# Optimization experiments

Hardware: AMD Instinct MI355X
Metric: run time of the kernel (lower is better)

## Reference

```python
import jax, jax.numpy as jnp
import numpy as np

N, E, IN, H, D = 50000, 800000, 128, 2, 64  # nodes, edges, in_dim, heads, out_dim per head
EPS = 1e-16  # PyG softmax denominator epsilon


def setup_inputs() -> dict:
    key = jax.random.key(0)
    ks = jax.random.split(key, 10)
    s = 1.0 / np.sqrt(IN)
    u = lambda k, shape: jax.random.uniform(k, shape, jnp.float32, -s, s)
    return {
        "x": jax.random.normal(ks[0], (N, IN), jnp.float32),
        "edge_index": jax.random.randint(ks[1], (2, E), 0, N, jnp.int64),
        "Wq": u(ks[2], (IN, H * D)), "bq": u(ks[3], (H * D,)),
        "Wk": u(ks[4], (IN, H * D)), "bk": u(ks[5], (H * D,)),
        "Wv": u(ks[6], (IN, H * D)), "bv": u(ks[7], (H * D,)),
        "Ws": u(ks[8], (IN, H * D)), "bs": u(ks[9], (H * D,)),
    }


def reference(x, edge_index, Wq, bq, Wk, bk, Wv, bv, Ws, bs):
    src, dst = edge_index[0], edge_index[1]
    # node-level projections [N, H, D]
    q = (x @ Wq + bq).reshape(N, H, D)
    k = (x @ Wk + bk).reshape(N, H, D)
    v = (x @ Wv + bv).reshape(N, H, D)
    # per-edge attention logits [E, H]
    alpha = jnp.einsum('ehd,ehd->eh', q[dst], k[src]) / np.float32(np.sqrt(D))
    # segment softmax over incoming edges of each dst node
    amax = jax.ops.segment_max(alpha, dst, num_segments=N)      # [N, H]
    amax = jnp.where(jnp.isfinite(amax), amax, 0.0)
    ealpha = jnp.exp(alpha - amax[dst])                          # [E, H]
    denom = jax.ops.segment_sum(ealpha, dst, num_segments=N)     # [N, H]
    w = ealpha / (denom[dst] + EPS)                              # [E, H]
    # scatter-aggregate weighted values -> [N, H, D]
    agg = jax.ops.segment_sum(w[:, :, None] * v[src], dst, num_segments=N)
    out = agg.reshape(N, H * D) + (x @ Ws + bs)                  # root/skip term
    return jax.nn.relu(out)
```

## Files before the change

kernel.cpp:

```cpp
#include <hip/hip_runtime.h>
#include <hip/hip_bf16.h>


#define N_NODES 50000
#define E_EDGES 800000
#define IN_DIM  128
#define HD      128
#define NPB     256
#define NB      196
#define EB      2048
#define NBLK_AC ((E_EDGES + EB - 1) / EB)
#define NTILES  ((N_NODES + 63) / 64)
#define PBLK    256
#define PSCALE  0.18033688011112042f

typedef float  f32x4  __attribute__((ext_vector_type(4)));
typedef float  f32x2  __attribute__((ext_vector_type(2)));
typedef __bf16 bf16x8 __attribute__((ext_vector_type(8)));
typedef unsigned short u16x8 __attribute__((ext_vector_type(8)));

__device__ __forceinline__ float bf2f(unsigned short u) {
    return __uint_as_float((unsigned int)u << 16);
}

__global__ __launch_bounds__(512) void proj_kernel(
    const float* __restrict__ x,
    const float* __restrict__ Wq, const float* __restrict__ bq,
    const float* __restrict__ Wk, const float* __restrict__ bk,
    const float* __restrict__ Wv, const float* __restrict__ bv,
    const float* __restrict__ Ws, const float* __restrict__ bs,
    __bf16* __restrict__ qb, unsigned char* __restrict__ kv8,
    __bf16* __restrict__ sbuf)
{
    __shared__ __bf16 xs[64][136];

    const int tid  = threadIdx.x;
    const int lane = tid & 63;
    const int wave = tid >> 6;
    const int l15  = lane & 15;
    const int g    = lane >> 4;

    const int p    = wave >> 1;
    const int colh = (wave & 1) * 64;
    const float* Wp     = (p == 0) ? Wq : (p == 1) ? Wk : (p == 2) ? Wv : Ws;
    const float* bias_p = (p == 0) ? bq : (p == 1) ? bk : (p == 2) ? bv : bs;

    bf16x8 Bf[4][4];
    #pragma unroll
    for (int ks = 0; ks < 4; ++ks) {
        #pragma unroll
        for (int cf = 0; cf < 4; ++cf) {
            bf16x8 b;
            #pragma unroll
            for (int j = 0; j < 8; ++j)
                b[j] = (__bf16)Wp[(size_t)(ks * 32 + g * 8 + j) * HD + colh + cf * 16 + l15];
            Bf[ks][cf] = b;
        }
    }

    float bias_v[4];
    #pragma unroll
    for (int cf = 0; cf < 4; ++cf) bias_v[cf] = bias_p[colh + cf * 16 + l15];

    const int srow = tid >> 5;
    const int sc4  = tid & 31;

    int t = blockIdx.x;
    float4 pre[4];
    if (t < NTILES) {
        #pragma unroll
        for (int it = 0; it < 4; ++it) {
            int row  = it * 16 + srow;
            int grow = t * 64 + row;
            pre[it] = (grow < N_NODES) ? *(const float4*)(x + (size_t)grow * IN_DIM + sc4 * 4)
                                       : make_float4(0.f, 0.f, 0.f, 0.f);
        }
    }

    for (; t < NTILES; t += PBLK) {
        __syncthreads();
        #pragma unroll
        for (int it = 0; it < 4; ++it) {
            int row = it * 16 + srow;
            __bf16* dst = &xs[row][sc4 * 4];
            dst[0] = (__bf16)pre[it].x; dst[1] = (__bf16)pre[it].y;
            dst[2] = (__bf16)pre[it].z; dst[3] = (__bf16)pre[it].w;
        }
        __syncthreads();

        int tn = t + PBLK;
        if (tn < NTILES) {
            #pragma unroll
            for (int it = 0; it < 4; ++it) {
                int row  = it * 16 + srow;
                int grow = tn * 64 + row;
                pre[it] = (grow < N_NODES) ? *(const float4*)(x + (size_t)grow * IN_DIM + sc4 * 4)
                                           : make_float4(0.f, 0.f, 0.f, 0.f);
            }
        }

        f32x4 acc[4][4];
        #pragma unroll
        for (int i = 0; i < 4; ++i)
            #pragma unroll
            for (int j = 0; j < 4; ++j) acc[i][j] = (f32x4){0.f, 0.f, 0.f, 0.f};

        #pragma unroll
        for (int ks = 0; ks < 4; ++ks) {
            #pragma unroll
            for (int rf = 0; rf < 4; ++rf) {
                bf16x8 A = *(const bf16x8*)&xs[rf * 16 + l15][ks * 32 + g * 8];
                #pragma unroll
                for (int cf = 0; cf < 4; ++cf)
                    acc[rf][cf] = __builtin_amdgcn_mfma_f32_16x16x32_bf16(A, Bf[ks][cf], acc[rf][cf], 0, 0, 0);
            }
        }

        const int nodebase = t * 64;
        if (p == 0 || p == 3) {
            __bf16* outp = (p == 0) ? qb : sbuf;
            #pragma unroll
            for (int cf = 0; cf < 4; ++cf) {
                int col = colh + cf * 16 + l15;
                #pragma unroll
                for (int rf = 0; rf < 4; ++rf) {
                    #pragma unroll
                    for (int r = 0; r < 4; ++r) {
                        int grow = nodebase + rf * 16 + g * 4 + r;
                        if (grow < N_NODES)
                            outp[(size_t)grow * HD + col] = (__bf16)(acc[rf][cf][r] + bias_v[cf]);
                    }
                }
            }
        } else {
            unsigned char* outp = kv8 + ((p == 2) ? 128 : 0);
            #pragma unroll
            for (int cf = 0; cf < 4; ++cf) {
                int col = colh + cf * 16 + l15;
                #pragma unroll
                for (int rf = 0; rf < 4; ++rf) {
                    #pragma unroll
                    for (int r = 0; r < 4; ++r) {
                        int grow = nodebase + rf * 16 + g * 4 + r;
                        if (grow < N_NODES) {
                            float val = acc[rf][cf][r] + bias_v[cf];
                            unsigned int pk = __builtin_amdgcn_cvt_pk_fp8_f32(val, val, 0, false);
                            outp[(size_t)grow * 256 + col] = (unsigned char)(pk & 0xff);
                        }
                    }
                }
            }
        }
    }
}

__global__ __launch_bounds__(256) void histA(
    const int* __restrict__ ei, int* __restrict__ hist)
{
    __shared__ int h[NB];
    const int tid = threadIdx.x;
    for (int i = tid; i < NB; i += 256) h[i] = 0;
    __syncthreads();

    const int* dsts = ei + E_EDGES;
    const int base = blockIdx.x * EB;
    #pragma unroll
    for (int half = 0; half < 2; ++half) {
        int e0 = base + half * 1024 + tid * 4;
        if (e0 + 3 < E_EDGES) {
            int4 d = *(const int4*)(dsts + e0);
            atomicAdd(&h[d.x >> 8], 1);
            atomicAdd(&h[d.y >> 8], 1);
            atomicAdd(&h[d.z >> 8], 1);
            atomicAdd(&h[d.w >> 8], 1);
        } else {
            for (int j = 0; j < 4; ++j)
                if (e0 + j < E_EDGES) atomicAdd(&h[dsts[e0 + j] >> 8], 1);
        }
    }
    __syncthreads();
    for (int i = tid; i < NB; i += 256)
        hist[i * NBLK_AC + blockIdx.x] = h[i];
}

__global__ __launch_bounds__(256) void scanB1(
    int* __restrict__ hist, int* __restrict__ sums)
{
    __shared__ int a[512];
    const int tid = threadIdx.x;
    const int b   = blockIdx.x;
    int* hb = hist + (size_t)b * NBLK_AC;

    a[tid]       = (tid       < NBLK_AC) ? hb[tid]       : 0;
    a[tid + 256] = (tid + 256 < NBLK_AC) ? hb[tid + 256] : 0;
    __syncthreads();
    #pragma unroll
    for (int d = 1; d < 512; d <<= 1) {
        int v0 = a[tid],       u0 = (tid       >= d) ? a[tid - d]       : 0;
        int v1 = a[tid + 256], u1 = (tid + 256 >= d) ? a[tid + 256 - d] : 0;
        __syncthreads();
        a[tid] = v0 + u0; a[tid + 256] = v1 + u1;
        __syncthreads();
    }
    if (tid < NBLK_AC)       hb[tid]       = (tid == 0) ? 0 : a[tid - 1];
    if (tid + 256 < NBLK_AC) hb[tid + 256] = a[tid + 255];
    if (tid == 0) sums[b] = a[NBLK_AC - 1];
}

__global__ __launch_bounds__(256) void scanB2(
    const int* __restrict__ sums, int* __restrict__ binbase)
{
    __shared__ int a[256];
    const int tid = threadIdx.x;
    a[tid] = (tid < NB) ? sums[tid] : 0;
    __syncthreads();
    #pragma unroll
    for (int d = 1; d < 256; d <<= 1) {
        int v = a[tid];
        int u = (tid >= d) ? a[tid - d] : 0;
        __syncthreads();
        a[tid] = v + u;
        __syncthreads();
    }
    if (tid < NB) binbase[tid] = (tid == 0) ? 0 : a[tid - 1];
    if (tid == 0) binbase[NB] = a[255];
}

__global__ __launch_bounds__(256) void scatterC(
    const int* __restrict__ ei, const int* __restrict__ hist,
    const int* __restrict__ binbase, int2* __restrict__ part)
{
    __shared__ int hb[NB];
    __shared__ int h2[NB];
    const int tid = threadIdx.x;
    for (int i = tid; i < NB; i += 256) {
        hb[i] = hist[i * NBLK_AC + blockIdx.x] + binbase[i];
        h2[i] = 0;
    }
    __syncthreads();

    const int* srcs = ei;
    const int* dsts = ei + E_EDGES;
    const int base = blockIdx.x * EB;
    #pragma unroll
    for (int half = 0; half < 2; ++half) {
        int e0 = base + half * 1024 + tid * 4;
        if (e0 + 3 < E_EDGES) {
            int4 s4 = *(const int4*)(srcs + e0);
            int4 d4 = *(const int4*)(dsts + e0);
            int bin, r;
            bin = d4.x >> 8; r = atomicAdd(&h2[bin], 1); part[hb[bin] + r] = make_int2(s4.x, d4.x);
            bin = d4.y >> 8; r = atomicAdd(&h2[bin], 1); part[hb[bin] + r] = make_int2(s4.y, d4.y);
            bin = d4.z >> 8; r = atomicAdd(&h2[bin], 1); part[hb[bin] + r] = make_int2(s4.z, d4.z);
            bin = d4.w >> 8; r = atomicAdd(&h2[bin], 1); part[hb[bin] + r] = make_int2(s4.w, d4.w);
        } else {
            for (int j = 0; j < 4; ++j) {
                if (e0 + j < E_EDGES) {
                    int sv = srcs[e0 + j], dv = dsts[e0 + j];
                    int bin = dv >> 8;
                    int r = atomicAdd(&h2[bin], 1);
                    part[hb[bin] + r] = make_int2(sv, dv);
                }
            }
        }
    }
}

__global__ __launch_bounds__(256) void buildD(
    const int2* __restrict__ part, const int* __restrict__ binbase,
    int* __restrict__ slot, int* __restrict__ nbase)
{
    __shared__ int cnt2[NPB];
    __shared__ int pfx[NPB];
    __shared__ int ofs[NPB];
    const int tid = threadIdx.x;
    const int b   = blockIdx.x;
    const int lo  = binbase[b];
    const int hi  = binbase[b + 1];
    const int n0  = b * NPB;

    cnt2[tid] = 0;
    __syncthreads();
    for (int i = lo + tid; i < hi; i += 256)
        atomicAdd(&cnt2[part[i].y - n0], 1);
    __syncthreads();

    pfx[tid] = cnt2[tid];
    __syncthreads();
    #pragma unroll
    for (int d = 1; d < NPB; d <<= 1) {
        int v = pfx[tid];
        int u = (tid >= d) ? pfx[tid - d] : 0;
        __syncthreads();
        pfx[tid] = v + u;
        __syncthreads();
    }
    const int excl = pfx[tid] - cnt2[tid];
    ofs[tid] = excl;
    const int node = n0 + tid;
    if (node < N_NODES) nbase[node] = lo + excl;
    if (b == NB - 1 && tid == 0) nbase[N_NODES] = E_EDGES;
    __syncthreads();

    for (int i = lo + tid; i < hi; i += 256) {
        int2 e = part[i];
        int r = atomicAdd(&ofs[e.y - n0], 1);
        slot[lo + r] = e.x;
    }
}

__global__ __launch_bounds__(256) void aggregate_kernel(
    const __bf16* __restrict__ qb, const unsigned char* __restrict__ kv8,
    const __bf16* __restrict__ sbuf,
    const int* __restrict__ nbase, const int* __restrict__ slot,
    float* __restrict__ out)
{
    const int tid  = threadIdx.x;
    const int lane = tid & 63;
    const int wave = tid >> 6;
    const int h    = lane >> 5;
    const int lh   = lane & 31;
    const int s    = lh >> 4;
    const int l16  = lh & 15;
    const int node = blockIdx.x * 8 + wave * 2 + h;
    const bool nvalid = node < N_NODES;
    const int nc = nvalid ? node : 0;

    const int bse = nbase[nc];
    const int deg = nvalid ? (nbase[nc + 1] - bse) : 0;

    u16x8 qu = *(const u16x8*)(qb + (size_t)nc * HD + 8 * l16);
    float qf[8];
    #pragma unroll
    for (int c = 0; c < 8; ++c) qf[c] = bf2f(qu[c]);

    float lsum = 0.f;
    float acc[8];
    #pragma unroll
    for (int c = 0; c < 8; ++c) acc[c] = 0.f;

    for (int i = 0; i < deg; i += 8) {
        int  jj[4], se[4];
        uint2 kr[4], vr[4];
        float d[4];

        #pragma unroll
        for (int r = 0; r < 4; ++r) {
            jj[r] = i + 2 * r + s;
            int sv = slot[bse + ((jj[r] < deg) ? jj[r] : 0)];
            se[r] = (jj[r] < deg) ? sv : 0;
        }
        #pragma unroll
        for (int r = 0; r < 4; ++r) {
            const unsigned char* rowp = kv8 + (size_t)se[r] * 256 + 8 * l16;
            kr[r] = *(const uint2*)rowp;
            vr[r] = *(const uint2*)(rowp + 128);
        }
        #pragma unroll
        for (int r = 0; r < 4; ++r) {
            f32x2 ka = __builtin_amdgcn_cvt_pk_f32_fp8(kr[r].x, 0);
            f32x2 kb_ = __builtin_amdgcn_cvt_pk_f32_fp8(kr[r].x, 1);
            f32x2 kc = __builtin_amdgcn_cvt_pk_f32_fp8(kr[r].y, 0);
            f32x2 kd = __builtin_amdgcn_cvt_pk_f32_fp8(kr[r].y, 1);
            d[r] = qf[0] * ka.x + qf[1] * ka.y + qf[2] * kb_.x + qf[3] * kb_.y
                 + qf[4] * kc.x + qf[5] * kc.y + qf[6] * kd.x + qf[7] * kd.y;
        }
        #pragma unroll
        for (int m = 1; m <= 4; m <<= 1) {
            d[0] += __shfl_xor(d[0], m);
            d[1] += __shfl_xor(d[1], m);
            d[2] += __shfl_xor(d[2], m);
            d[3] += __shfl_xor(d[3], m);
        }
        #pragma unroll
        for (int r = 0; r < 4; ++r) {
            float a2 = (jj[r] < deg) ? d[r] * PSCALE : -INFINITY;
            float p  = exp2f(a2);
            lsum += p;
            f32x2 va = __builtin_amdgcn_cvt_pk_f32_fp8(vr[r].x, 0);
            f32x2 vb_ = __builtin_amdgcn_cvt_pk_f32_fp8(vr[r].x, 1);
            f32x2 vc = __builtin_amdgcn_cvt_pk_f32_fp8(vr[r].y, 0);
            f32x2 vd = __builtin_amdgcn_cvt_pk_f32_fp8(vr[r].y, 1);
            acc[0] += p * va.x;  acc[1] += p * va.y;
            acc[2] += p * vb_.x; acc[3] += p * vb_.y;
            acc[4] += p * vc.x;  acc[5] += p * vc.y;
            acc[6] += p * vd.x;  acc[7] += p * vd.y;
        }
    }

    lsum += __shfl_xor(lsum, 16);
    #pragma unroll
    for (int c = 0; c < 8; ++c) acc[c] += __shfl_xor(acc[c], 16);

    float inv = (deg > 0) ? 1.f / (lsum + 1e-16f) : 0.f;
    u16x8 su = *(const u16x8*)(sbuf + (size_t)nc * HD + 8 * l16);

    f32x4 ov;
    #pragma unroll
    for (int cc = 0; cc < 4; ++cc) {
        float av;
        unsigned short sv;
        switch (cc) {
            case 0: av = s ? acc[4] : acc[0]; sv = s ? su[4] : su[0]; break;
            case 1: av = s ? acc[5] : acc[1]; sv = s ? su[5] : su[1]; break;
            case 2: av = s ? acc[6] : acc[2]; sv = s ? su[6] : su[2]; break;
            default: av = s ? acc[7] : acc[3]; sv = s ? su[7] : su[3]; break;
        }
        ov[cc] = fmaxf(av * inv + bf2f(sv), 0.f);
    }
    if (nvalid)
        *(f32x4*)(out + (size_t)node * HD + 8 * l16 + 4 * s) = ov;
}

extern "C" void kernel_launch(void* const* d_in, const int* in_sizes, int n_in,
                              void* d_out, int out_size, void* d_ws, size_t ws_size,
                              hipStream_t stream)
{
    const float* x  = (const float*)d_in[0];
    const int*   ei = (const int*)d_in[1];
    const float* Wq = (const float*)d_in[2];
    const float* bq = (const float*)d_in[3];
    const float* Wk = (const float*)d_in[4];
    const float* bk = (const float*)d_in[5];
    const float* Wv = (const float*)d_in[6];
    const float* bv = (const float*)d_in[7];
    const float* Ws = (const float*)d_in[8];
    const float* bs = (const float*)d_in[9];

    char* ws = (char*)d_ws;
    size_t off = 0;
    auto alloc = [&](size_t bytes) {
        void* p = ws + off;
        off += (bytes + 255) & ~(size_t)255;
        return p;
    };
    const size_t projB = (size_t)N_NODES * HD * sizeof(__bf16);
    __bf16* qb = (__bf16*)alloc(projB);
    unsigned char* kv8 = (unsigned char*)alloc((size_t)N_NODES * 256);
    __bf16* sbf = (__bf16*)alloc(projB);
    int* hist    = (int*)alloc((size_t)NB * NBLK_AC * sizeof(int));
    int* sums    = (int*)alloc((size_t)NB * sizeof(int));
    int* binbase = (int*)alloc((size_t)(NB + 1) * sizeof(int));
    int2* part   = (int2*)alloc((size_t)E_EDGES * sizeof(int2));
    int* slot    = (int*)alloc((size_t)E_EDGES * sizeof(int));
    int* nbase   = (int*)alloc((size_t)(N_NODES + 1) * sizeof(int));

    histA<<<NBLK_AC, 256, 0, stream>>>(ei, hist);
    scanB1<<<NB, 256, 0, stream>>>(hist, sums);
    scanB2<<<1, 256, 0, stream>>>(sums, binbase);
    scatterC<<<NBLK_AC, 256, 0, stream>>>(ei, hist, binbase, part);
    buildD<<<NB, 256, 0, stream>>>(part, binbase, slot, nbase);

    proj_kernel<<<PBLK, 512, 0, stream>>>(
        x, Wq, bq, Wk, bk, Wv, bv, Ws, bs, qb, kv8, sbf);

    aggregate_kernel<<<(N_NODES + 7) / 8, 256, 0, stream>>>(
        qb, kv8, sbf, nbase, slot, (float*)d_out);
}
```

Baseline: 90.97 us.

## Restructure projection into single-wave blocks with pre-transposed bf16 weights

Adds a small kernel that transposes all four weight matrices to bf16 so each wave can load its B fragments as vector loads instead of 8 strided scalar fp32 loads. The projection kernel becomes 4096 one-wave blocks, each owning one projection/column-half role. Each wave reads 16-row x tiles straight from global memory into registers, with no LDS staging and no barriers. The cost is that every x tile is now read by 8 different waves instead of once per block, which leans on L2, and it adds an extra kernel launch.

```diff
diff --git a/kernel.cpp b/kernel.cpp
--- a/kernel.cpp
+++ b/kernel.cpp
@@ -10,8 +10,8 @@
 #define NB      196
 #define EB      2048
 #define NBLK_AC ((E_EDGES + EB - 1) / EB)
-#define NTILES  ((N_NODES + 63) / 64)
-#define PBLK    256
+#define NT16    (N_NODES / 16)
+#define PWAVES  4096
 #define PSCALE  0.18033688011112042f
 
 typedef float  f32x4  __attribute__((ext_vector_type(4)));
@@ -23,113 +23,81 @@
     return __uint_as_float((unsigned int)u << 16);
 }
 
-__global__ __launch_bounds__(512) void proj_kernel(
-    const float* __restrict__ x,
-    const float* __restrict__ Wq, const float* __restrict__ bq,
-    const float* __restrict__ Wk, const float* __restrict__ bk,
-    const float* __restrict__ Wv, const float* __restrict__ bv,
-    const float* __restrict__ Ws, const float* __restrict__ bs,
+__global__ __launch_bounds__(256) void wtrans_kernel(
+    const float* __restrict__ Wq, const float* __restrict__ Wk,
+    const float* __restrict__ Wv, const float* __restrict__ Ws,
+    __bf16* __restrict__ WT)
+{
+    int idx = blockIdx.x * 256 + threadIdx.x;
+    int p   = idx >> 14;
+    int rem = idx & 16383;
+    int k   = rem >> 7;
+    int col = rem & 127;
+    const float* W = (p == 0) ? Wq : (p == 1) ? Wk : (p == 2) ? Wv : Ws;
+    WT[(size_t)p * 16384 + col * 128 + k] = (__bf16)W[k * HD + col];
+}
+
+__global__ __launch_bounds__(64) void proj_kernel(
+    const float* __restrict__ x, const __bf16* __restrict__ WT,
+    const float* __restrict__ bq, const float* __restrict__ bk,
+    const float* __restrict__ bv, const float* __restrict__ bs,
     __bf16* __restrict__ qb, unsigned char* __restrict__ kv8,
     __bf16* __restrict__ sbuf)
 {
-    __shared__ __bf16 xs[64][136];
-
-    const int tid  = threadIdx.x;
-    const int lane = tid & 63;
-    const int wave = tid >> 6;
+    const int lane = threadIdx.x & 63;
     const int l15  = lane & 15;
     const int g    = lane >> 4;
 
-    const int p    = wave >> 1;
-    const int colh = (wave & 1) * 64;
-    const float* Wp     = (p == 0) ? Wq : (p == 1) ? Wk : (p == 2) ? Wv : Ws;
+    const int role = blockIdx.x & 7;
+    const int p    = role >> 1;
+    const int colh = (role & 1) * 64;
+
     const float* bias_p = (p == 0) ? bq : (p == 1) ? bk : (p == 2) ? bv : bs;
+    const __bf16* WTp = WT + ((size_t)p * 128 + colh) * 128;
 
     bf16x8 Bf[4][4];
     #pragma unroll
-    for (int ks = 0; ks < 4; ++ks) {
-        #pragma unroll
-        for (int cf = 0; cf < 4; ++cf) {
-            bf16x8 b;
+    for (int ks = 0; ks < 4; ++ks)
+        #pragma unroll
+        for (int cf = 0; cf < 4; ++cf)
+            Bf[ks][cf] = *(const bf16x8*)(WTp + (size_t)(cf * 16 + l15) * 128 + ks * 32 + g * 8);
+
+    float bias_v[4];
+    #pragma unroll
+    for (int cf = 0; cf < 4; ++cf) bias_v[cf] = bias_p[colh + cf * 16 + l15];
+
+    for (int t = blockIdx.x >> 3; t < NT16; t += (PWAVES >> 3)) {
+        const float* xrow = x + (size_t)(t * 16 + l15) * IN_DIM;
+
+        bf16x8 A[4];
+        #pragma unroll
+        for (int ks = 0; ks < 4; ++ks) {
+            f32x4 a0 = *(const f32x4*)(xrow + ks * 32 + g * 8);
+            f32x4 a1 = *(const f32x4*)(xrow + ks * 32 + g * 8 + 4);
+            bf16x8 a;
+            a[0] = (__bf16)a0.x; a[1] = (__bf16)a0.y; a[2] = (__bf16)a0.z; a[3] = (__bf16)a0.w;
+            a[4] = (__bf16)a1.x; a[5] = (__bf16)a1.y; a[6] = (__bf16)a1.z; a[7] = (__bf16)a1.w;
+            A[ks] = a;
+        }
+
+        f32x4 acc[4];
+        #pragma unroll
+        for (int cf = 0; cf < 4; ++cf) acc[cf] = (f32x4){0.f, 0.f, 0.f, 0.f};
+        #pragma unroll
+        for (int ks = 0; ks < 4; ++ks)
             #pragma unroll
-            for (int j = 0; j < 8; ++j)
-                b[j] = (__bf16)Wp[(size_t)(ks * 32 + g * 8 + j) * HD + colh + cf * 16 + l15];
-            Bf[ks][cf] = b;
-        }
-    }
-
-    float bias_v[4];
-    #pragma unroll
-    for (int cf = 0; cf < 4; ++cf) bias_v[cf] = bias_p[colh + cf * 16 + l15];
-
-    const int srow = tid >> 5;
-    const int sc4  = tid & 31;
-
-    int t = blockIdx.x;
-    float4 pre[4];
-    if (t < NTILES) {
-        #pragma unroll
-        for (int it = 0; it < 4; ++it) {
-            int row  = it * 16 + srow;
-            int grow = t * 64 + row;
-            pre[it] = (grow < N_NODES) ? *(const float4*)(x + (size_t)grow * IN_DIM + sc4 * 4)
-                                       : make_float4(0.f, 0.f, 0.f, 0.f);
-        }
-    }
-
-    for (; t < NTILES; t += PBLK) {
-        __syncthreads();
-        #pragma unroll
-        for (int it = 0; it < 4; ++it) {
-            int row = it * 16 + srow;
-            __bf16* dst = &xs[row][sc4 * 4];
-            dst[0] = (__bf16)pre[it].x; dst[1] = (__bf16)pre[it].y;
-            dst[2] = (__bf16)pre[it].z; dst[3] = (__bf16)pre[it].w;
-        }
-        __syncthreads();
-
-        int tn = t + PBLK;
-        if (tn < NTILES) {
-            #pragma unroll
-            for (int it = 0; it < 4; ++it) {
-                int row  = it * 16 + srow;
-                int grow = tn * 64 + row;
-                pre[it] = (grow < N_NODES) ? *(const float4*)(x + (size_t)grow * IN_DIM + sc4 * 4)
-                                           : make_float4(0.f, 0.f, 0.f, 0.f);
-            }
-        }
-
-        f32x4 acc[4][4];
-        #pragma unroll
-        for (int i = 0; i < 4; ++i)
-            #pragma unroll
-            for (int j = 0; j < 4; ++j) acc[i][j] = (f32x4){0.f, 0.f, 0.f, 0.f};
-
-        #pragma unroll
-        for (int ks = 0; ks < 4; ++ks) {
-            #pragma unroll
-            for (int rf = 0; rf < 4; ++rf) {
-                bf16x8 A = *(const bf16x8*)&xs[rf * 16 + l15][ks * 32 + g * 8];
-                #pragma unroll
-                for (int cf = 0; cf < 4; ++cf)
-                    acc[rf][cf] = __builtin_amdgcn_mfma_f32_16x16x32_bf16(A, Bf[ks][cf], acc[rf][cf], 0, 0, 0);
-            }
-        }
-
-        const int nodebase = t * 64;
+            for (int cf = 0; cf < 4; ++cf)
+                acc[cf] = __builtin_amdgcn_mfma_f32_16x16x32_bf16(A[ks], Bf[ks][cf], acc[cf], 0, 0, 0);
+
         if (p == 0 || p == 3) {
             __bf16* outp = (p == 0) ? qb : sbuf;
             #pragma unroll
             for (int cf = 0; cf < 4; ++cf) {
                 int col = colh + cf * 16 + l15;
                 #pragma unroll
-                for (int rf = 0; rf < 4; ++rf) {
-                    #pragma unroll
-                    for (int r = 0; r < 4; ++r) {
-                        int grow = nodebase + rf * 16 + g * 4 + r;
-                        if (grow < N_NODES)
-                            outp[(size_t)grow * HD + col] = (__bf16)(acc[rf][cf][r] + bias_v[cf]);
-                    }
+                for (int r = 0; r < 4; ++r) {
+                    int node = t * 16 + g * 4 + r;
+                    outp[(size_t)node * HD + col] = (__bf16)(acc[cf][r] + bias_v[cf]);
                 }
             }
         } else {
@@ -138,16 +106,11 @@
             for (int cf = 0; cf < 4; ++cf) {
                 int col = colh + cf * 16 + l15;
                 #pragma unroll
-                for (int rf = 0; rf < 4; ++rf) {
-                    #pragma unroll
-                    for (int r = 0; r < 4; ++r) {
-                        int grow = nodebase + rf * 16 + g * 4 + r;
-                        if (grow < N_NODES) {
-                            float val = acc[rf][cf][r] + bias_v[cf];
-                            unsigned int pk = __builtin_amdgcn_cvt_pk_fp8_f32(val, val, 0, false);
-                            outp[(size_t)grow * 256 + col] = (unsigned char)(pk & 0xff);
-                        }
-                    }
+                for (int r = 0; r < 4; ++r) {
+                    int node = t * 16 + g * 4 + r;
+                    float val = acc[cf][r] + bias_v[cf];
+                    unsigned int pk = __builtin_amdgcn_cvt_pk_fp8_f32(val, val, 0, false);
+                    outp[(size_t)node * 256 + col] = (unsigned char)(pk & 0xff);
                 }
             }
         }
@@ -438,6 +401,7 @@
     __bf16* qb = (__bf16*)alloc(projB);
     unsigned char* kv8 = (unsigned char*)alloc((size_t)N_NODES * 256);
     __bf16* sbf = (__bf16*)alloc(projB);
+    __bf16* WT  = (__bf16*)alloc((size_t)4 * 128 * 128 * sizeof(__bf16));
     int* hist    = (int*)alloc((size_t)NB * NBLK_AC * sizeof(int));
     int* sums    = (int*)alloc((size_t)NB * sizeof(int));
     int* binbase = (int*)alloc((size_t)(NB + 1) * sizeof(int));
@@ -451,8 +415,10 @@
     scatterC<<<NBLK_AC, 256, 0, stream>>>(ei, hist, binbase, part);
     buildD<<<NB, 256, 0, stream>>>(part, binbase, slot, nbase);
 
-    proj_kernel<<<PBLK, 512, 0, stream>>>(
-        x, Wq, bq, Wk, bk, Wv, bv, Ws, bs, qb, kv8, sbf);
+    wtrans_kernel<<<256, 256, 0, stream>>>(Wq, Wk, Wv, Ws, WT);
+
+    proj_kernel<<<PWAVES, 64, 0, stream>>>(
+        x, WT, bq, bk, bv, bs, qb, kv8, sbf);
 
     aggregate_kernel<<<(N_NODES + 7) / 8, 256, 0, stream>>>(
         qb, kv8, sbf, nbase, slot, (float*)d_out);
```

After: 112.9 us. 24.1% more time.

## Launch one projection block per 128-node tile instead of persistent grid-stride blocks

Applied to the files above, without the earlier changes.

The projection kernel drops its persistent 256-block grid-stride loop with register prefetch. It now launches one block per 128-node tile (391 blocks), loads the whole tile into shared memory once, and processes 16-row fragments one at a time with a 4-accumulator set. This spreads work over more CUs and cuts accumulator register pressure. In exchange, every block reloads and converts the full weight fragments from global memory, and the load of x no longer overlaps with compute.

```diff
diff --git a/kernel.cpp b/kernel.cpp
--- a/kernel.cpp
+++ b/kernel.cpp
@@ -10,8 +10,7 @@
 #define NB      196
 #define EB      2048
 #define NBLK_AC ((E_EDGES + EB - 1) / EB)
-#define NTILES  ((N_NODES + 63) / 64)
-#define PBLK    256
+#define NT128   ((N_NODES + 127) / 128)
 #define PSCALE  0.18033688011112042f
 
 typedef float  f32x4  __attribute__((ext_vector_type(4)));
@@ -32,7 +31,7 @@
     __bf16* __restrict__ qb, unsigned char* __restrict__ kv8,
     __bf16* __restrict__ sbuf)
 {
-    __shared__ __bf16 xs[64][136];
+    __shared__ __bf16 xs[128][136];
 
     const int tid  = threadIdx.x;
     const int lane = tid & 63;
@@ -62,74 +61,47 @@
     #pragma unroll
     for (int cf = 0; cf < 4; ++cf) bias_v[cf] = bias_p[colh + cf * 16 + l15];
 
+    const int nodebase = blockIdx.x * 128;
     const int srow = tid >> 5;
     const int sc4  = tid & 31;
-
-    int t = blockIdx.x;
-    float4 pre[4];
-    if (t < NTILES) {
-        #pragma unroll
-        for (int it = 0; it < 4; ++it) {
-            int row  = it * 16 + srow;
-            int grow = t * 64 + row;
-            pre[it] = (grow < N_NODES) ? *(const float4*)(x + (size_t)grow * IN_DIM + sc4 * 4)
-                                       : make_float4(0.f, 0.f, 0.f, 0.f);
-        }
-    }
-
-    for (; t < NTILES; t += PBLK) {
-        __syncthreads();
-        #pragma unroll
-        for (int it = 0; it < 4; ++it) {
-            int row = it * 16 + srow;
-            __bf16* dst = &xs[row][sc4 * 4];
-            dst[0] = (__bf16)pre[it].x; dst[1] = (__bf16)pre[it].y;
-            dst[2] = (__bf16)pre[it].z; dst[3] = (__bf16)pre[it].w;
-        }
-        __syncthreads();
-
-        int tn = t + PBLK;
-        if (tn < NTILES) {
+    #pragma unroll
+    for (int it = 0; it < 8; ++it) {
+        int row  = it * 16 + srow;
+        int grow = nodebase + row;
+        float4 v = (grow < N_NODES) ? *(const float4*)(x + (size_t)grow * IN_DIM + sc4 * 4)
+                                    : make_float4(0.f, 0.f, 0.f, 0.f);
+        __bf16* dst = &xs[row][sc4 * 4];
+        dst[0] = (__bf16)v.x; dst[1] = (__bf16)v.y;
+        dst[2] = (__bf16)v.z; dst[3] = (__bf16)v.w;
+    }
+    __syncthreads();
+
+    #pragma unroll
+    for (int rf = 0; rf < 8; ++rf) {
+        bf16x8 A[4];
+        #pragma unroll
+        for (int ks = 0; ks < 4; ++ks)
+            A[ks] = *(const bf16x8*)&xs[rf * 16 + l15][ks * 32 + g * 8];
+
+        f32x4 acc[4];
+        #pragma unroll
+        for (int cf = 0; cf < 4; ++cf) acc[cf] = (f32x4){0.f, 0.f, 0.f, 0.f};
+        #pragma unroll
+        for (int ks = 0; ks < 4; ++ks)
             #pragma unroll
-            for (int it = 0; it < 4; ++it) {
-                int row  = it * 16 + srow;
-                int grow = tn * 64 + row;
-                pre[it] = (grow < N_NODES) ? *(const float4*)(x + (size_t)grow * IN_DIM + sc4 * 4)
-                                           : make_float4(0.f, 0.f, 0.f, 0.f);
-            }
-        }
-
-        f32x4 acc[4][4];
-        #pragma unroll
-        for (int i = 0; i < 4; ++i)
-            #pragma unroll
-            for (int j = 0; j < 4; ++j) acc[i][j] = (f32x4){0.f, 0.f, 0.f, 0.f};
-
-        #pragma unroll
-        for (int ks = 0; ks < 4; ++ks) {
-            #pragma unroll
-            for (int rf = 0; rf < 4; ++rf) {
-                bf16x8 A = *(const bf16x8*)&xs[rf * 16 + l15][ks * 32 + g * 8];
-                #pragma unroll
-                for (int cf = 0; cf < 4; ++cf)
-                    acc[rf][cf] = __builtin_amdgcn_mfma_f32_16x16x32_bf16(A, Bf[ks][cf], acc[rf][cf], 0, 0, 0);
-            }
-        }
-
-        const int nodebase = t * 64;
+            for (int cf = 0; cf < 4; ++cf)
+                acc[cf] = __builtin_amdgcn_mfma_f32_16x16x32_bf16(A[ks], Bf[ks][cf], acc[cf], 0, 0, 0);
+
         if (p == 0 || p == 3) {
             __bf16* outp = (p == 0) ? qb : sbuf;
             #pragma unroll
             for (int cf = 0; cf < 4; ++cf) {
                 int col = colh + cf * 16 + l15;
                 #pragma unroll
-                for (int rf = 0; rf < 4; ++rf) {
-                    #pragma unroll
-                    for (int r = 0; r < 4; ++r) {
-                        int grow = nodebase + rf * 16 + g * 4 + r;
-                        if (grow < N_NODES)
-                            outp[(size_t)grow * HD + col] = (__bf16)(acc[rf][cf][r] + bias_v[cf]);
-                    }
+                for (int r = 0; r < 4; ++r) {
+                    int grow = nodebase + rf * 16 + g * 4 + r;
+                    if (grow < N_NODES)
+                        outp[(size_t)grow * HD + col] = (__bf16)(acc[cf][r] + bias_v[cf]);
                 }
             }
         } else {
@@ -138,15 +110,12 @@
             for (int cf = 0; cf < 4; ++cf) {
                 int col = colh + cf * 16 + l15;
                 #pragma unroll
-                for (int rf = 0; rf < 4; ++rf) {
-                    #pragma unroll
-                    for (int r = 0; r < 4; ++r) {
-                        int grow = nodebase + rf * 16 + g * 4 + r;
-                        if (grow < N_NODES) {
-                            float val = acc[rf][cf][r] + bias_v[cf];
-                            unsigned int pk = __builtin_amdgcn_cvt_pk_fp8_f32(val, val, 0, false);
-                            outp[(size_t)grow * 256 + col] = (unsigned char)(pk & 0xff);
-                        }
+                for (int r = 0; r < 4; ++r) {
+                    int grow = nodebase + rf * 16 + g * 4 + r;
+                    if (grow < N_NODES) {
+                        float val = acc[cf][r] + bias_v[cf];
+                        unsigned int pk = __builtin_amdgcn_cvt_pk_fp8_f32(val, val, 0, false);
+                        outp[(size_t)grow * 256 + col] = (unsigned char)(pk & 0xff);
                     }
                 }
             }
@@ -451,7 +420,7 @@
     scatterC<<<NBLK_AC, 256, 0, stream>>>(ei, hist, binbase, part);
     buildD<<<NB, 256, 0, stream>>>(part, binbase, slot, nbase);
 
-    proj_kernel<<<PBLK, 512, 0, stream>>>(
+    proj_kernel<<<NT128, 512, 0, stream>>>(
         x, Wq, bq, Wk, bk, Wv, bv, Ws, bs, qb, kv8, sbf);
 
     aggregate_kernel<<<(N_NODES + 7) / 8, 256, 0, stream>>>(
```

After: 104.5 us. 1.15x slower.
